# Optimization experiments

Measured on AMD Instinct MI355X. Metric: run time of the kernel, lower is better.

Reference implementation:

```python
import jax, jax.numpy as jnp
import numpy as np

HIDDEN, FFN, N_EXPERTS, TOP_K = 1024, 2816, 8, 2


def setup_inputs() -> dict:
    key = jax.random.key(0)
    k1, k2, k3, k4, k5 = jax.random.split(key, 5)
    hidden_states = jax.random.normal(k1, (1, 2048, HIDDEN), dtype=jnp.float32)
    # torch Linear weights: [out, in]; experts stacked on leading E axis
    Wgate = jax.random.normal(k2, (N_EXPERTS, HIDDEN), dtype=jnp.float32) * 0.02
    Wg = jax.random.normal(k3, (N_EXPERTS, FFN, HIDDEN), dtype=jnp.float32) * 0.02
    Wu = jax.random.normal(k4, (N_EXPERTS, FFN, HIDDEN), dtype=jnp.float32) * 0.02
    Wd = jax.random.normal(k5, (N_EXPERTS, HIDDEN, FFN), dtype=jnp.float32) * 0.02
    return {"hidden_states": hidden_states, "Wgate": Wgate, "Wg": Wg, "Wu": Wu, "Wd": Wd}


def reference(hidden_states, Wgate, Wg, Wu, Wd):
    x = hidden_states.reshape(-1, hidden_states.shape[-1])  # [T, H]
    # --- router ---
    logits = jnp.einsum('th,eh->te', x, Wgate)               # [T, E]
    weights = jax.nn.softmax(logits, axis=-1)
    topk_w, topk_i = jax.lax.top_k(weights, TOP_K)           # [T, K]
    topk_w = topk_w / jnp.sum(topk_w, axis=-1, keepdims=True)
    # per-token per-expert combine weight (zero if expert not in top-k)
    comb = jnp.sum(jax.nn.one_hot(topk_i, N_EXPERTS, dtype=x.dtype) * topk_w[..., None], axis=1)  # [T, E]
    # --- all-expert SwiGLU (dense reference for the gather-compute-scatter loop) ---
    g = jnp.einsum('th,efh->tef', x, Wg)                     # [T, E, F]
    u = jnp.einsum('th,efh->tef', x, Wu)
    h = jax.nn.silu(g) * u
    y = jnp.einsum('tef,ehf->teh', h, Wd)                    # [T, E, H]
    out = jnp.einsum('te,teh->th', comb, y)                  # [T, H]
    return out
```

## Files before the change

kernel.cpp:

```cpp
#include <hip/hip_runtime.h>
#include <hip/hip_bf16.h>

#define HIDDEN 1024
#define FFN    2816
#define NEXP   8
#define NTOK   2048

typedef __attribute__((ext_vector_type(8))) short short8;
typedef __attribute__((ext_vector_type(4))) float f32x4;

static __device__ __forceinline__ short f2bf(float f) {
    __hip_bfloat16 h = __float2bfloat16(f);
    return *(short*)&h;
}

static __device__ __forceinline__ void gl_lds16(const short* g, short* l) {
    __builtin_amdgcn_global_load_lds(
        (const __attribute__((address_space(1))) void*)g,
        (__attribute__((address_space(3))) void*)l, 16, 0, 0);
}

#define WAITV(N) asm volatile("s_waitcnt vmcnt(" #N ")" ::: "memory")
#define BAR()    do { __builtin_amdgcn_s_barrier(); \
                      __builtin_amdgcn_sched_barrier(0); } while (0)

__global__ void __launch_bounds__(64)
router_kernel(const float* __restrict__ x, const float* __restrict__ Wgate,
              int* __restrict__ counts, int* __restrict__ tok,
              float* __restrict__ wts)
{
    int t = blockIdx.x;
    int lane = threadIdx.x;
    float acc[NEXP];
#pragma unroll
    for (int e = 0; e < NEXP; e++) acc[e] = 0.f;
    const float* xrow = x + (size_t)t * HIDDEN;
    for (int h = lane; h < HIDDEN; h += 64) {
        float xv = xrow[h];
#pragma unroll
        for (int e = 0; e < NEXP; e++) acc[e] += xv * Wgate[e * HIDDEN + h];
    }
#pragma unroll
    for (int off = 32; off > 0; off >>= 1) {
#pragma unroll
        for (int e = 0; e < NEXP; e++) acc[e] += __shfl_down(acc[e], off);
    }
    if (lane == 0) {
        float mx = acc[0];
#pragma unroll
        for (int e = 1; e < NEXP; e++) mx = fmaxf(mx, acc[e]);
        float p[NEXP];
#pragma unroll
        for (int e = 0; e < NEXP; e++) p[e] = __expf(acc[e] - mx);
        int i0 = 0; float p0 = p[0];
#pragma unroll
        for (int e = 1; e < NEXP; e++) if (p[e] > p0) { p0 = p[e]; i0 = e; }
        int i1 = -1; float p1 = -1.f;
#pragma unroll
        for (int e = 0; e < NEXP; e++) {
            if (e == i0) continue;
            if (p[e] > p1) { p1 = p[e]; i1 = e; }
        }
        float inv = 1.f / (p0 + p1);
        float w0 = p0 * inv, w1 = p1 * inv;
        int s0 = atomicAdd(&counts[i0], 1);
        tok[i0 * NTOK + s0] = t; wts[i0 * NTOK + s0] = w0;
        int s1 = atomicAdd(&counts[i1], 1);
        tok[i1 * NTOK + s1] = t; wts[i1 * NTOK + s1] = w1;
    }
}

__global__ void __launch_bounds__(256)
cvt_all(const float* __restrict__ s0, const float* __restrict__ s1,
        const float* __restrict__ s2, const float* __restrict__ s3,
        short* __restrict__ d0, short* __restrict__ d1,
        short* __restrict__ d2, short* __restrict__ d3)
{
    const long long n0 = (long long)(NTOK * HIDDEN) / 8;
    const long long nw = (long long)NEXP * FFN * HIDDEN / 8;
    long long tot = n0 + 3 * nw;
    for (long long i = (long long)blockIdx.x * 256 + threadIdx.x; i < tot;
         i += (long long)gridDim.x * 256) {
        const float* s; short* d; long long r;
        if (i < n0)               { s = s0; d = d0; r = i; }
        else if (i < n0 + nw)     { s = s1; d = d1; r = i - n0; }
        else if (i < n0 + 2 * nw) { s = s2; d = d2; r = i - n0 - nw; }
        else                      { s = s3; d = d3; r = i - n0 - 2 * nw; }
        float4 a = ((const float4*)s)[2 * r];
        float4 b = ((const float4*)s)[2 * r + 1];
        short8 o;
        o[0] = f2bf(a.x); o[1] = f2bf(a.y); o[2] = f2bf(a.z); o[3] = f2bf(a.w);
        o[4] = f2bf(b.x); o[5] = f2bf(b.y); o[6] = f2bf(b.z); o[7] = f2bf(b.w);
        *(short8*)(d + 8 * r) = o;
    }
}

__global__ void __launch_bounds__(256, 2)
ffn1_v4(const short* __restrict__ xbf, const short* __restrict__ Wgbf,
        const short* __restrict__ Wubf, const int* __restrict__ counts,
        const int* __restrict__ tok, short* __restrict__ hbuf)
{
    int bid = blockIdx.x;
    int xb  = bid / 176;
    int yz  = bid - xb * 176;
    int e   = yz / 22;
    int fb  = yz - e * 22;
    int cnt = counts[e];
    int row0 = xb * 128;
    if (row0 >= cnt) return;
    int off_e = 0;
#pragma unroll
    for (int i = 0; i < NEXP; i++) if (i < e) off_e += counts[i];
    int f0 = fb * 128;

    __shared__ short Xs[3][128 * 32];
    __shared__ short Gs[3][128 * 32];
    __shared__ short Us[3][128 * 32];
    __shared__ int   stok[128];

    int tid = threadIdx.x;
    if (tid < 128) stok[tid] = tok[e * NTOK + min(row0 + tid, cnt - 1)];
    __syncthreads();

    int lane = tid & 63, w = tid >> 6;
    int l15 = lane & 15, lq = lane >> 4;
    int wm = (w & 1) * 64, wn = (w >> 1) * 64;

    int prow   = lane >> 2;
    int gchunk = (lane & 3) ^ ((lane >> 3) & 3);
    const short* xsrc[2]; const short* gsrc[2]; const short* usrc[2];
    int rb[2];
#pragma unroll
    for (int j = 0; j < 2; j++) {
        int rbase = w * 32 + j * 16;
        int r = rbase + prow;
        xsrc[j] = xbf + (size_t)stok[r] * HIDDEN + gchunk * 8;
        gsrc[j] = Wgbf + (size_t)e * FFN * HIDDEN + (size_t)(f0 + r) * HIDDEN + gchunk * 8;
        usrc[j] = Wubf + (size_t)e * FFN * HIDDEN + (size_t)(f0 + r) * HIDDEN + gchunk * 8;
        rb[j] = rbase * 32;
    }

    int aoff[4], boff[4];
#pragma unroll
    for (int mi = 0; mi < 4; mi++) {
        int r = wm + mi * 16 + l15;
        aoff[mi] = r * 32 + (lq ^ ((r >> 1) & 3)) * 8;
    }
#pragma unroll
    for (int ni = 0; ni < 4; ni++) {
        int r = wn + ni * 16 + l15;
        boff[ni] = r * 32 + (lq ^ ((r >> 1) & 3)) * 8;
    }

    f32x4 cg[4][4], cu[4][4];
#pragma unroll
    for (int i = 0; i < 4; i++)
#pragma unroll
        for (int j = 0; j < 4; j++) { cg[i][j] = (f32x4)0.f; cu[i][j] = (f32x4)0.f; }

#define STAGE1(B, T) do { int _k = (T) * 32;                       \
    _Pragma("unroll")                                              \
    for (int j = 0; j < 2; j++) {                                  \
        gl_lds16(xsrc[j] + _k, &Xs[B][rb[j]]);                     \
        gl_lds16(gsrc[j] + _k, &Gs[B][rb[j]]);                     \
        gl_lds16(usrc[j] + _k, &Us[B][rb[j]]);                     \
    } } while (0)

#define COMP1(B) do {                                              \
    short8 af[4], bg[4], bu[4];                                    \
    _Pragma("unroll")                                              \
    for (int mi = 0; mi < 4; mi++)                                 \
        af[mi] = *(const short8*)&Xs[B][aoff[mi]];                 \
    _Pragma("unroll")                                              \
    for (int ni = 0; ni < 4; ni++) {                               \
        bg[ni] = *(const short8*)&Gs[B][boff[ni]];                 \
        bu[ni] = *(const short8*)&Us[B][boff[ni]];                 \
    }                                                              \
    _Pragma("unroll")                                              \
    for (int mi = 0; mi < 4; mi++)                                 \
    _Pragma("unroll")                                              \
    for (int ni = 0; ni < 4; ni++) {                               \
        cg[mi][ni] = __builtin_amdgcn_mfma_f32_16x16x32_bf16(af[mi], bg[ni], cg[mi][ni], 0, 0, 0); \
        cu[mi][ni] = __builtin_amdgcn_mfma_f32_16x16x32_bf16(af[mi], bu[ni], cu[mi][ni], 0, 0, 0); \
    } } while (0)

    STAGE1(0, 0); STAGE1(1, 1); STAGE1(2, 2);

    for (int tt = 0; tt < 30; tt += 3) {
        WAITV(12); BAR(); COMP1(0); BAR(); STAGE1(0, tt + 3);
        WAITV(12); BAR(); COMP1(1); BAR(); STAGE1(1, tt + 4);
        WAITV(12); BAR(); COMP1(2); BAR(); if (tt + 5 < 32) STAGE1(2, tt + 5);
    }
    WAITV(6);  BAR(); COMP1(0);
    WAITV(0);  BAR(); COMP1(1);

#undef STAGE1
#undef COMP1

#pragma unroll
    for (int mi = 0; mi < 4; mi++)
#pragma unroll
        for (int r = 0; r < 4; r++) {
            int row = wm + mi * 16 + lq * 4 + r;
            int grow = row0 + row;
            if (grow < cnt) {
                short* hrow = hbuf + (size_t)(off_e + grow) * FFN + f0 + wn;
#pragma unroll
                for (int ni = 0; ni < 4; ni++) {
                    float g = cg[mi][ni][r], u = cu[mi][ni][r];
                    float h = g / (1.f + __expf(-g)) * u;
                    hrow[ni * 16 + l15] = f2bf(h);
                }
            }
        }
}

__global__ void __launch_bounds__(256, 2)
ffn2_v4(const short* __restrict__ hbuf, const short* __restrict__ Wdbf,
        const int* __restrict__ counts, const int* __restrict__ tok,
        const float* __restrict__ wts, float* __restrict__ out)
{
    int bid = blockIdx.x;
    int xb  = bid >> 7;
    int yz  = bid & 127;
    int e   = yz >> 4;
    int y   = yz & 15;
    int cnt = counts[e];
    int row0 = xb * 128;
    if (row0 >= cnt) return;
    int off_e = 0;
#pragma unroll
    for (int i = 0; i < NEXP; i++) if (i < e) off_e += counts[i];
    int h0    = (y >> 1) * 128;
    int kbase = (y & 1) * (FFN / 2);

    __shared__ short Hs[3][128 * 32];
    __shared__ short Ds[3][128 * 32];
    __shared__ int   stok[128];
    __shared__ float swt[128];

    int tid = threadIdx.x;
    if (tid < 128) {
        int rc = min(row0 + tid, cnt - 1);
        stok[tid] = tok[e * NTOK + rc];
        swt[tid]  = wts[e * NTOK + rc];
    }
    __syncthreads();

    int lane = tid & 63, w = tid >> 6;
    int l15 = lane & 15, lq = lane >> 4;
    int wm = (w & 1) * 64, wn = (w >> 1) * 64;

    int prow   = lane >> 2;
    int gchunk = (lane & 3) ^ ((lane >> 3) & 3);
    const short* hsrc[2]; const short* dsrc[2];
    int rb[2];
#pragma unroll
    for (int j = 0; j < 2; j++) {
        int rbase = w * 32 + j * 16;
        int r = rbase + prow;
        hsrc[j] = hbuf + (size_t)(off_e + min(row0 + r, cnt - 1)) * FFN + kbase + gchunk * 8;
        dsrc[j] = Wdbf + (size_t)e * HIDDEN * FFN + (size_t)(h0 + r) * FFN + kbase + gchunk * 8;
        rb[j] = rbase * 32;
    }

    int aoff[4], boff[4];
#pragma unroll
    for (int mi = 0; mi < 4; mi++) {
        int r = wm + mi * 16 + l15;
        aoff[mi] = r * 32 + (lq ^ ((r >> 1) & 3)) * 8;
    }
#pragma unroll
    for (int ni = 0; ni < 4; ni++) {
        int r = wn + ni * 16 + l15;
        boff[ni] = r * 32 + (lq ^ ((r >> 1) & 3)) * 8;
    }

    f32x4 c[4][4];
#pragma unroll
    for (int i = 0; i < 4; i++)
#pragma unroll
        for (int j = 0; j < 4; j++) c[i][j] = (f32x4)0.f;

#define STAGE2(B, T) do { int _k = (T) * 32;                       \
    _Pragma("unroll")                                              \
    for (int j = 0; j < 2; j++) {                                  \
        gl_lds16(hsrc[j] + _k, &Hs[B][rb[j]]);                     \
        gl_lds16(dsrc[j] + _k, &Ds[B][rb[j]]);                     \
    } } while (0)

#define COMP2(B) do {                                              \
    short8 af[4], bd[4];                                           \
    _Pragma("unroll")                                              \
    for (int mi = 0; mi < 4; mi++)                                 \
        af[mi] = *(const short8*)&Hs[B][aoff[mi]];                 \
    _Pragma("unroll")                                              \
    for (int ni = 0; ni < 4; ni++)                                 \
        bd[ni] = *(const short8*)&Ds[B][boff[ni]];                 \
    _Pragma("unroll")                                              \
    for (int mi = 0; mi < 4; mi++)                                 \
    _Pragma("unroll")                                              \
    for (int ni = 0; ni < 4; ni++)                                 \
        c[mi][ni] = __builtin_amdgcn_mfma_f32_16x16x32_bf16(af[mi], bd[ni], c[mi][ni], 0, 0, 0); \
    } while (0)

    STAGE2(0, 0); STAGE2(1, 1); STAGE2(2, 2);

    for (int tt = 0; tt < 42; tt += 3) {
        WAITV(8); BAR(); COMP2(0); BAR(); STAGE2(0, tt + 3);
        WAITV(8); BAR(); COMP2(1); BAR(); STAGE2(1, tt + 4);
        WAITV(8); BAR(); COMP2(2); BAR(); if (tt + 5 < 44) STAGE2(2, tt + 5);
    }
    WAITV(4); BAR(); COMP2(0);
    WAITV(0); BAR(); COMP2(1);

#undef STAGE2
#undef COMP2

#pragma unroll
    for (int mi = 0; mi < 4; mi++)
#pragma unroll
        for (int r = 0; r < 4; r++) {
            int row = wm + mi * 16 + lq * 4 + r;
            int grow = row0 + row;
            if (grow < cnt) {
                int t = stok[row];
                float wgt = swt[row];
                float* orow = out + (size_t)t * HIDDEN + h0 + wn;
#pragma unroll
                for (int ni = 0; ni < 4; ni++)
                    atomicAdd(&orow[ni * 16 + l15], wgt * c[mi][ni][r]);
            }
        }
}

#define LDW 40
__global__ void __launch_bounds__(256, 2)
ffn1_fb(const float* __restrict__ x, const float* __restrict__ Wg,
        const float* __restrict__ Wu, const int* __restrict__ counts,
        const int* __restrict__ tok, __hip_bfloat16* __restrict__ hbuf)
{
    int e = blockIdx.z;
    int cnt = counts[e];
    int row0 = blockIdx.x * 128;
    if (row0 >= cnt) return;
    int off_e = 0;
#pragma unroll
    for (int i = 0; i < NEXP; i++) if (i < e) off_e += counts[i];
    int f0 = blockIdx.y * 64;

    __shared__ short Xs[128][LDW];
    __shared__ short Gs[64][LDW];
    __shared__ short Us[64][LDW];
    __shared__ int   stok[128];

    int tid = threadIdx.x;
    if (tid < 128) stok[tid] = tok[e * NTOK + min(row0 + tid, cnt - 1)];
    __syncthreads();

    int lane = tid & 63, w = tid >> 6;
    int wm = (w & 1) * 64, wn = (w >> 1) * 32;
    int l15 = lane & 15, lq = lane >> 4;

    f32x4 cg[4][2], cu[4][2];
#pragma unroll
    for (int i = 0; i < 4; i++)
#pragma unroll
        for (int j = 0; j < 2; j++) { cg[i][j] = (f32x4)0.f; cu[i][j] = (f32x4)0.f; }

    const float* Wge = Wg + (size_t)e * FFN * HIDDEN;
    const float* Wue = Wu + (size_t)e * FFN * HIDDEN;

    int xr[4], xc[4]; const float* xp[4];
#pragma unroll
    for (int i = 0; i < 4; i++) {
        int idx = tid + 256 * i;
        xr[i] = idx >> 3; xc[i] = (idx & 7) * 4;
        xp[i] = x + (size_t)stok[xr[i]] * HIDDEN + xc[i];
    }
    int wr[2], wc[2]; const float* gp[2]; const float* up[2];
#pragma unroll
    for (int i = 0; i < 2; i++) {
        int idx = tid + 256 * i;
        wr[i] = idx >> 3; wc[i] = (idx & 7) * 4;
        gp[i] = Wge + (size_t)(f0 + wr[i]) * HIDDEN + wc[i];
        up[i] = Wue + (size_t)(f0 + wr[i]) * HIDDEN + wc[i];
    }

    float4 xa[4], ga[2], ua[2];
#pragma unroll
    for (int i = 0; i < 4; i++) xa[i] = *(const float4*)(xp[i]);
#pragma unroll
    for (int i = 0; i < 2; i++) { ga[i] = *(const float4*)(gp[i]); ua[i] = *(const float4*)(up[i]); }

    for (int k0 = 0; k0 < HIDDEN; k0 += 32) {
        __syncthreads();
#pragma unroll
        for (int i = 0; i < 4; i++) {
            short* d = &Xs[xr[i]][xc[i]];
            d[0] = f2bf(xa[i].x); d[1] = f2bf(xa[i].y);
            d[2] = f2bf(xa[i].z); d[3] = f2bf(xa[i].w);
        }
#pragma unroll
        for (int i = 0; i < 2; i++) {
            short* d = &Gs[wr[i]][wc[i]];
            d[0] = f2bf(ga[i].x); d[1] = f2bf(ga[i].y);
            d[2] = f2bf(ga[i].z); d[3] = f2bf(ga[i].w);
            short* d2 = &Us[wr[i]][wc[i]];
            d2[0] = f2bf(ua[i].x); d2[1] = f2bf(ua[i].y);
            d2[2] = f2bf(ua[i].z); d2[3] = f2bf(ua[i].w);
        }
        __syncthreads();
        if (k0 + 32 < HIDDEN) {
            int kn = k0 + 32;
#pragma unroll
            for (int i = 0; i < 4; i++) xa[i] = *(const float4*)(xp[i] + kn);
#pragma unroll
            for (int i = 0; i < 2; i++) { ga[i] = *(const float4*)(gp[i] + kn); ua[i] = *(const float4*)(up[i] + kn); }
        }
        short8 af[4], bg[2], bu[2];
#pragma unroll
        for (int mi = 0; mi < 4; mi++) af[mi] = *(const short8*)&Xs[wm + mi * 16 + l15][lq * 8];
#pragma unroll
        for (int ni = 0; ni < 2; ni++) {
            bg[ni] = *(const short8*)&Gs[wn + ni * 16 + l15][lq * 8];
            bu[ni] = *(const short8*)&Us[wn + ni * 16 + l15][lq * 8];
        }
#pragma unroll
        for (int mi = 0; mi < 4; mi++)
#pragma unroll
            for (int ni = 0; ni < 2; ni++) {
                cg[mi][ni] = __builtin_amdgcn_mfma_f32_16x16x32_bf16(af[mi], bg[ni], cg[mi][ni], 0, 0, 0);
                cu[mi][ni] = __builtin_amdgcn_mfma_f32_16x16x32_bf16(af[mi], bu[ni], cu[mi][ni], 0, 0, 0);
            }
    }

#pragma unroll
    for (int mi = 0; mi < 4; mi++)
#pragma unroll
        for (int r = 0; r < 4; r++) {
            int row = wm + mi * 16 + lq * 4 + r;
            int grow = row0 + row;
            if (grow < cnt) {
                __hip_bfloat16* hrow = hbuf + (size_t)(off_e + grow) * FFN + f0 + wn;
#pragma unroll
                for (int ni = 0; ni < 2; ni++) {
                    float g = cg[mi][ni][r], u = cu[mi][ni][r];
                    float h = g / (1.f + __expf(-g)) * u;
                    hrow[ni * 16 + l15] = __float2bfloat16(h);
                }
            }
        }
}

__global__ void __launch_bounds__(256, 2)
ffn2_fb(const __hip_bfloat16* __restrict__ hbuf, const float* __restrict__ Wd,
        const int* __restrict__ counts, const int* __restrict__ tok,
        const float* __restrict__ wts, float* __restrict__ out)
{
    int e = blockIdx.z;
    int cnt = counts[e];
    int row0 = blockIdx.x * 128;
    if (row0 >= cnt) return;
    int off_e = 0;
#pragma unroll
    for (int i = 0; i < NEXP; i++) if (i < e) off_e += counts[i];
    int h0 = blockIdx.y * 64;

    __shared__ short Hs[128][LDW];
    __shared__ short Ds[64][LDW];
    __shared__ int   stok[128];
    __shared__ float swt[128];

    int tid = threadIdx.x;
    if (tid < 128) {
        int rc = min(row0 + tid, cnt - 1);
        stok[tid] = tok[e * NTOK + rc];
        swt[tid]  = wts[e * NTOK + rc];
    }
    __syncthreads();

    int lane = tid & 63, w = tid >> 6;
    int wm = (w & 1) * 64, wn = (w >> 1) * 32;
    int l15 = lane & 15, lq = lane >> 4;

    f32x4 c[4][2];
#pragma unroll
    for (int i = 0; i < 4; i++)
#pragma unroll
        for (int j = 0; j < 2; j++) c[i][j] = (f32x4)0.f;

    const float* Wde = Wd + (size_t)e * HIDDEN * FFN;

    int hr[2], hc[2]; const short* hp[2];
#pragma unroll
    for (int i = 0; i < 2; i++) {
        int idx = tid + 256 * i;
        hr[i] = idx >> 2; hc[i] = (idx & 3) * 8;
        int ar = min(row0 + hr[i], cnt - 1);
        hp[i] = (const short*)(hbuf + (size_t)(off_e + ar) * FFN + hc[i]);
    }
    int dr[2], dc[2]; const float* dp[2];
#pragma unroll
    for (int i = 0; i < 2; i++) {
        int idx = tid + 256 * i;
        dr[i] = idx >> 3; dc[i] = (idx & 7) * 4;
        dp[i] = Wde + (size_t)(h0 + dr[i]) * FFN + dc[i];
    }

    short8 ha[2]; float4 da[2];
#pragma unroll
    for (int i = 0; i < 2; i++) { ha[i] = *(const short8*)(hp[i]); da[i] = *(const float4*)(dp[i]); }

    for (int k0 = 0; k0 < FFN; k0 += 32) {
        __syncthreads();
#pragma unroll
        for (int i = 0; i < 2; i++) {
            *(short8*)&Hs[hr[i]][hc[i]] = ha[i];
            short* d = &Ds[dr[i]][dc[i]];
            d[0] = f2bf(da[i].x); d[1] = f2bf(da[i].y);
            d[2] = f2bf(da[i].z); d[3] = f2bf(da[i].w);
        }
        __syncthreads();
        if (k0 + 32 < FFN) {
            int kn = k0 + 32;
#pragma unroll
            for (int i = 0; i < 2; i++) { ha[i] = *(const short8*)(hp[i] + kn); da[i] = *(const float4*)(dp[i] + kn); }
        }
        short8 af[4], bf_[2];
#pragma unroll
        for (int mi = 0; mi < 4; mi++) af[mi] = *(const short8*)&Hs[wm + mi * 16 + l15][lq * 8];
#pragma unroll
        for (int ni = 0; ni < 2; ni++) bf_[ni] = *(const short8*)&Ds[wn + ni * 16 + l15][lq * 8];
#pragma unroll
        for (int mi = 0; mi < 4; mi++)
#pragma unroll
            for (int ni = 0; ni < 2; ni++)
                c[mi][ni] = __builtin_amdgcn_mfma_f32_16x16x32_bf16(af[mi], bf_[ni], c[mi][ni], 0, 0, 0);
    }

#pragma unroll
    for (int mi = 0; mi < 4; mi++)
#pragma unroll
        for (int r = 0; r < 4; r++) {
            int row = wm + mi * 16 + lq * 4 + r;
            int grow = row0 + row;
            if (grow < cnt) {
                int t = stok[row];
                float wgt = swt[row];
                float* orow = out + (size_t)t * HIDDEN + h0 + wn;
#pragma unroll
                for (int ni = 0; ni < 2; ni++)
                    atomicAdd(&orow[ni * 16 + l15], wgt * c[mi][ni][r]);
            }
        }
}

extern "C" void kernel_launch(void* const* d_in, const int* in_sizes, int n_in,
                              void* d_out, int out_size, void* d_ws, size_t ws_size,
                              hipStream_t stream) {
    const float* x     = (const float*)d_in[0];
    const float* Wgate = (const float*)d_in[1];
    const float* Wg    = (const float*)d_in[2];
    const float* Wu    = (const float*)d_in[3];
    const float* Wd    = (const float*)d_in[4];
    float* out = (float*)d_out;

    char* ws = (char*)d_ws;
    int*   counts = (int*)ws;
    int*   tok    = (int*)(ws + 256);
    float* wts    = (float*)(ws + 256 + NEXP * NTOK * 4);

    hipMemsetAsync(counts, 0, 256, stream);
    hipMemsetAsync(out, 0, (size_t)out_size * sizeof(float), stream);

    router_kernel<<<NTOK, 64, 0, stream>>>(x, Wgate, counts, tok, wts);

    const size_t base = 256 + 2 * (size_t)NEXP * NTOK * 4;
    const size_t NEED = base
        + 2ull * NTOK * HIDDEN
        + 3ull * 2ull * NEXP * FFN * HIDDEN
        + 2ull * 2ull * NTOK * FFN;

    if (ws_size >= NEED) {
        short* xbf  = (short*)(ws + base);
        short* wgbf = xbf  + (size_t)NTOK * HIDDEN;
        short* wubf = wgbf + (size_t)NEXP * FFN * HIDDEN;
        short* wdbf = wubf + (size_t)NEXP * FFN * HIDDEN;
        short* hbuf = wdbf + (size_t)NEXP * HIDDEN * FFN;

        cvt_all<<<8192, 256, 0, stream>>>(x, Wg, Wu, Wd, xbf, wgbf, wubf, wdbf);

        ffn1_v4<<<2816, 256, 0, stream>>>(xbf, wgbf, wubf, counts, tok, hbuf);
        ffn2_v4<<<2048, 256, 0, stream>>>(hbuf, wdbf, counts, tok, wts, out);
    } else {
        __hip_bfloat16* hbuf = (__hip_bfloat16*)(ws + base);
        dim3 g1(NTOK / 128, FFN / 64, NEXP);
        ffn1_fb<<<g1, 256, 0, stream>>>(x, Wg, Wu, counts, tok, hbuf);
        dim3 g2(NTOK / 128, HIDDEN / 64, NEXP);
        ffn2_fb<<<g2, 256, 0, stream>>>(hbuf, Wd, counts, tok, wts, out);
    }
}
```

Measured before the change: 482.1 us.

## Fuse router into bf16 conversion kernel and reorder FFN block indexing by expert

Merges the router into the weight/activation conversion kernel: the first 512 blocks each route four tokens with one wavefront per token, and the remaining blocks convert fp32 to bf16 four elements per thread in a fixed, non-grid-stride layout. This saves a kernel launch and lets routing overlap with the bandwidth-bound conversion. The FFN kernels now decode block IDs expert-major with the row block fastest, so blocks that share an expert's weight tile run close together and can reuse it in L2. The conversion uses narrower 8-byte stores and a very large grid, which may reduce store efficiency.

Measured after the change: 676.2 us. 1.4x slower.

```diff
diff --git a/kernel.cpp b/kernel.cpp
--- a/kernel.cpp
+++ b/kernel.cpp
@@ -7,6 +7,7 @@
 #define NTOK   2048
 
 typedef __attribute__((ext_vector_type(8))) short short8;
+typedef __attribute__((ext_vector_type(4))) short bf16x4;
 typedef __attribute__((ext_vector_type(4))) float f32x4;
 
 static __device__ __forceinline__ short f2bf(float f) {
@@ -24,13 +25,11 @@
 #define BAR()    do { __builtin_amdgcn_s_barrier(); \
                       __builtin_amdgcn_sched_barrier(0); } while (0)
 
-__global__ void __launch_bounds__(64)
-router_kernel(const float* __restrict__ x, const float* __restrict__ Wgate,
-              int* __restrict__ counts, int* __restrict__ tok,
-              float* __restrict__ wts)
+static __device__ __forceinline__ void
+router_body(int t, int lane, const float* __restrict__ x,
+            const float* __restrict__ Wgate, int* __restrict__ counts,
+            int* __restrict__ tok, float* __restrict__ wts)
 {
-    int t = blockIdx.x;
-    int lane = threadIdx.x;
     float acc[NEXP];
 #pragma unroll
     for (int e = 0; e < NEXP; e++) acc[e] = 0.f;
@@ -70,41 +69,59 @@
     }
 }
 
+__global__ void __launch_bounds__(64)
+router_kernel(const float* __restrict__ x, const float* __restrict__ Wgate,
+              int* __restrict__ counts, int* __restrict__ tok,
+              float* __restrict__ wts)
+{
+    router_body(blockIdx.x, threadIdx.x, x, Wgate, counts, tok, wts);
+}
+
+#define N04 ((long long)NTOK * HIDDEN / 4)
+#define NW4 ((long long)NEXP * FFN * HIDDEN / 4)
+#define CVT_BLOCKS 17408
 __global__ void __launch_bounds__(256)
-cvt_all(const float* __restrict__ s0, const float* __restrict__ s1,
-        const float* __restrict__ s2, const float* __restrict__ s3,
-        short* __restrict__ d0, short* __restrict__ d1,
-        short* __restrict__ d2, short* __restrict__ d3)
+fused_cvt_router(const float* __restrict__ x, const float* __restrict__ Wgate,
+                 int* __restrict__ counts, int* __restrict__ tok,
+                 float* __restrict__ wts,
+                 const float* __restrict__ s1, const float* __restrict__ s2,
+                 const float* __restrict__ s3,
+                 short* __restrict__ d0, short* __restrict__ d1,
+                 short* __restrict__ d2, short* __restrict__ d3)
 {
-    const long long n0 = (long long)(NTOK * HIDDEN) / 8;
-    const long long nw = (long long)NEXP * FFN * HIDDEN / 8;
-    long long tot = n0 + 3 * nw;
-    for (long long i = (long long)blockIdx.x * 256 + threadIdx.x; i < tot;
-         i += (long long)gridDim.x * 256) {
+    int bid = blockIdx.x;
+    int tid = threadIdx.x;
+    if (bid < 512) {
+        int t = bid * 4 + (tid >> 6);
+        router_body(t, tid & 63, x, Wgate, counts, tok, wts);
+        return;
+    }
+    long long base4 = (long long)(bid - 512) * 1024;
+#pragma unroll
+    for (int p = 0; p < 4; p++) {
+        long long i = base4 + p * 256 + tid;
         const float* s; short* d; long long r;
-        if (i < n0)               { s = s0; d = d0; r = i; }
-        else if (i < n0 + nw)     { s = s1; d = d1; r = i - n0; }
-        else if (i < n0 + 2 * nw) { s = s2; d = d2; r = i - n0 - nw; }
-        else                      { s = s3; d = d3; r = i - n0 - 2 * nw; }
-        float4 a = ((const float4*)s)[2 * r];
-        float4 b = ((const float4*)s)[2 * r + 1];
-        short8 o;
+        if (i < N04)               { s = x;  d = d0; r = i; }
+        else if (i < N04 + NW4)    { s = s1; d = d1; r = i - N04; }
+        else if (i < N04 + 2*NW4)  { s = s2; d = d2; r = i - N04 - NW4; }
+        else                       { s = s3; d = d3; r = i - N04 - 2*NW4; }
+        float4 a = ((const float4*)s)[r];
+        bf16x4 o;
         o[0] = f2bf(a.x); o[1] = f2bf(a.y); o[2] = f2bf(a.z); o[3] = f2bf(a.w);
-        o[4] = f2bf(b.x); o[5] = f2bf(b.y); o[6] = f2bf(b.z); o[7] = f2bf(b.w);
-        *(short8*)(d + 8 * r) = o;
+        *(bf16x4*)(d + 4 * r) = o;
     }
 }
 
 __global__ void __launch_bounds__(256, 2)
-ffn1_v4(const short* __restrict__ xbf, const short* __restrict__ Wgbf,
+ffn1_v5(const short* __restrict__ xbf, const short* __restrict__ Wgbf,
         const short* __restrict__ Wubf, const int* __restrict__ counts,
         const int* __restrict__ tok, short* __restrict__ hbuf)
 {
     int bid = blockIdx.x;
-    int xb  = bid / 176;
-    int yz  = bid - xb * 176;
-    int e   = yz / 22;
-    int fb  = yz - e * 22;
+    int e   = bid / 352;
+    int rem = bid - e * 352;
+    int fb  = rem >> 4;
+    int xb  = rem & 15;
     int cnt = counts[e];
     int row0 = xb * 128;
     if (row0 >= cnt) return;
@@ -216,15 +233,15 @@
 }
 
 __global__ void __launch_bounds__(256, 2)
-ffn2_v4(const short* __restrict__ hbuf, const short* __restrict__ Wdbf,
+ffn2_v5(const short* __restrict__ hbuf, const short* __restrict__ Wdbf,
         const int* __restrict__ counts, const int* __restrict__ tok,
         const float* __restrict__ wts, float* __restrict__ out)
 {
     int bid = blockIdx.x;
-    int xb  = bid >> 7;
-    int yz  = bid & 127;
-    int e   = yz >> 4;
-    int y   = yz & 15;
+    int e   = bid >> 8;
+    int rem = bid & 255;
+    int y   = rem >> 4;
+    int xb  = rem & 15;
     int cnt = counts[e];
     int row0 = xb * 128;
     if (row0 >= cnt) return;
@@ -574,8 +591,6 @@
     hipMemsetAsync(counts, 0, 256, stream);
     hipMemsetAsync(out, 0, (size_t)out_size * sizeof(float), stream);
 
-    router_kernel<<<NTOK, 64, 0, stream>>>(x, Wgate, counts, tok, wts);
-
     const size_t base = 256 + 2 * (size_t)NEXP * NTOK * 4;
     const size_t NEED = base
         + 2ull * NTOK * HIDDEN
@@ -589,11 +604,13 @@
         short* wdbf = wubf + (size_t)NEXP * FFN * HIDDEN;
         short* hbuf = wdbf + (size_t)NEXP * HIDDEN * FFN;
 
-        cvt_all<<<8192, 256, 0, stream>>>(x, Wg, Wu, Wd, xbf, wgbf, wubf, wdbf);
-
-        ffn1_v4<<<2816, 256, 0, stream>>>(xbf, wgbf, wubf, counts, tok, hbuf);
-        ffn2_v4<<<2048, 256, 0, stream>>>(hbuf, wdbf, counts, tok, wts, out);
+        fused_cvt_router<<<512 + CVT_BLOCKS, 256, 0, stream>>>(
+            x, Wgate, counts, tok, wts, Wg, Wu, Wd, xbf, wgbf, wubf, wdbf);
+
+        ffn1_v5<<<2816, 256, 0, stream>>>(xbf, wgbf, wubf, counts, tok, hbuf);
+        ffn2_v5<<<2048, 256, 0, stream>>>(hbuf, wdbf, counts, tok, wts, out);
     } else {
+        router_kernel<<<NTOK, 64, 0, stream>>>(x, Wgate, counts, tok, wts);
         __hip_bfloat16* hbuf = (__hip_bfloat16*)(ws + base);
         dim3 g1(NTOK / 128, FFN / 64, NEXP);
         ffn1_fb<<<g1, 256, 0, stream>>>(x, Wg, Wu, counts, tok, hbuf);
```
